# Optimization experiments

Hardware: AMD Instinct MI355X
Metric: run time of the kernel (lower is better)

## Reference

```python
import jax, jax.numpy as jnp
import numpy as np

G, N, E, F_IN, F_OUT, C = 256, 512, 4096, 64, 64, 16


def setup_inputs() -> dict:
    key = jax.random.key(0)
    ks = jax.random.split(key, 6)
    x_batch = jax.random.normal(ks[0], (G, N, F_IN), dtype=jnp.float32)
    edge_index_batch = jax.random.randint(ks[1], (G, 2, E), 0, N, dtype=jnp.int32)
    conv_weight = jax.random.normal(ks[2], (F_OUT, F_IN), dtype=jnp.float32) * (1.0 / np.sqrt(F_IN))
    conv_bias = jax.random.normal(ks[3], (F_OUT,), dtype=jnp.float32) * 0.02
    lin_weight = jax.random.normal(ks[4], (C, F_OUT * N), dtype=jnp.float32) * (1.0 / np.sqrt(F_OUT * N))
    lin_bias = jax.random.normal(ks[5], (C,), dtype=jnp.float32) * 0.02
    return {"x_batch": x_batch, "edge_index_batch": edge_index_batch,
            "conv_weight": conv_weight, "conv_bias": conv_bias,
            "lin_weight": lin_weight, "lin_bias": lin_bias}


def _gcn_conv_graph(xw, edge_index, self_loops):
    # xw: [N, F_OUT] (already linearly transformed), edge_index: [2, E]
    row = jnp.concatenate([edge_index[0], self_loops])  # sources
    col = jnp.concatenate([edge_index[1], self_loops])  # targets
    ones = jnp.ones(row.shape[0], dtype=xw.dtype)
    deg = jax.ops.segment_sum(ones, col, num_segments=N)  # degree at target nodes
    dinv = jnp.where(deg > 0, jax.lax.rsqrt(deg), jnp.zeros_like(deg))
    norm = dinv[row] * dinv[col]                          # [E+N]
    msgs = xw[row] * norm[:, None]                        # gather + normalize
    return jax.ops.segment_sum(msgs, col, num_segments=N)  # scatter-add at targets


def reference(x_batch, edge_index_batch, conv_weight, conv_bias, lin_weight, lin_bias):
    # GCNConv (PyG defaults: self-loops, symmetric normalization, post-agg bias)
    xw = jnp.einsum('gnf,of->gno', x_batch, conv_weight)  # [G, N, F_OUT]
    self_loops = jnp.arange(N, dtype=edge_index_batch.dtype)
    h = jax.vmap(_gcn_conv_graph, in_axes=(0, 0, None))(xw, edge_index_batch, self_loops)
    h = h + conv_bias
    h = jax.nn.relu(h)
    flat = h.reshape(h.shape[0], -1)                      # [G, N*F_OUT]
    logits = flat @ lin_weight.T + lin_bias               # [G, C]
    return jax.nn.log_softmax(logits, axis=-1)
```

## Files before the change

### kernel.cpp

```cpp
#include <hip/hip_runtime.h>

#define Gn 256
#define Nn 512
#define En 4096
#define Fn 64
#define Cn 16
#define ET (En + Nn)
#define EPAD 4616

typedef _Float16 halfv8 __attribute__((ext_vector_type(8)));
typedef _Float16 halfv4 __attribute__((ext_vector_type(4)));
typedef float    f32x4  __attribute__((ext_vector_type(4)));

__device__ __forceinline__ float pk_norm(unsigned p) {
    return (float)__builtin_bit_cast(_Float16, (unsigned short)(p & 0xffffu));
}

__global__ __launch_bounds__(256) void cvt_x(const float* __restrict__ x,
                                             _Float16* __restrict__ xc) {
    size_t base = (size_t)blockIdx.x * 256 + threadIdx.x;
    #pragma unroll
    for (int it = 0; it < 4; ++it) {
        size_t i = base + (size_t)it * (2048 * 256);
        float4 v = ((const float4*)x)[i];
        halfv4 h; h[0]=(_Float16)v.x; h[1]=(_Float16)v.y;
                  h[2]=(_Float16)v.z; h[3]=(_Float16)v.w;
        ((halfv4*)xc)[i] = h;
    }
}

__global__ __launch_bounds__(256) void cvt_lw_perm(const float* __restrict__ lw,
                                                   _Float16* __restrict__ lwh) {
    int u = blockIdx.x * 256 + threadIdx.x;
    int c = u >> 13, v = u & 8191;
    int jobidx = v >> 6, q = (v >> 4) & 3, m = v & 15;
    int n = (jobidx >> 2) * 16 + m;
    int o = (jobidx & 3) * 16 + q * 4;
    float4 f = *(const float4*)(lw + (size_t)c * (Nn * Fn) + n * 64 + o);
    halfv4 h; h[0]=(_Float16)f.x; h[1]=(_Float16)f.y;
              h[2]=(_Float16)f.z; h[3]=(_Float16)f.w;
    *(halfv4*)(lwh + (size_t)c * (Nn * Fn) + (size_t)v * 4) = h;
}

__global__ __launch_bounds__(256) void build_csr(const int* __restrict__ ei,
                                                 unsigned* __restrict__ epkG,
                                                 int* __restrict__ cntG) {
    __shared__ int      degL[Nn];
    __shared__ float    dinvL[Nn];
    __shared__ int      cntE[Nn];
    __shared__ unsigned epkL[ET];
    __shared__ int      wsum[4];
    const int g = blockIdx.x, tid = threadIdx.x;
    const int lane = tid & 63, wid = tid >> 6;
    const int* es = ei + (size_t)g * 2 * En;
    const int* ed = es + En;

    degL[tid] = 0; degL[tid + 256] = 0;
    __syncthreads();
    for (int e = tid; e < En; e += 256) atomicAdd(&degL[ed[e]], 1);
    __syncthreads();

    const int t2 = tid * 2;
    int cA = degL[t2] + 1, cB = degL[t2 + 1] + 1;
    dinvL[t2]     = rsqrtf((float)cA);
    dinvL[t2 + 1] = rsqrtf((float)cB);
    int p = cA + cB, v = p;
    #pragma unroll
    for (int off = 1; off < 64; off <<= 1) {
        int u = __shfl_up(v, off, 64);
        if (lane >= off) v += u;
    }
    if (lane == 63) wsum[wid] = v;
    __syncthreads();
    if (tid == 0) { int a = 0; for (int i = 0; i < 4; ++i) { int t = wsum[i]; wsum[i] = a; a += t; } }
    __syncthreads();
    int pe = v - p + wsum[wid];
    cntE[t2] = pe;
    cntE[t2 + 1] = pe + cA;
    __syncthreads();

    for (int e = tid; e < ET; e += 256) {
        int s, t;
        if (e < En) { s = es[e]; t = ed[e]; } else { s = t = e - En; }
        float nrm = dinvL[s] * dinvL[t];
        int slot = atomicAdd(&cntE[t], 1);
        unsigned short nb = __builtin_bit_cast(unsigned short, (_Float16)nrm);
        epkL[slot] = ((unsigned)s << 16) | nb;
    }
    __syncthreads();

    for (int i = tid; i < ET; i += 256) epkG[(size_t)g * EPAD + i] = epkL[i];
    cntG[(size_t)g * Nn + t2]     = cntE[t2];
    cntG[(size_t)g * Nn + t2 + 1] = cntE[t2 + 1];
}

__global__ __launch_bounds__(512, 4) void agg_conv(
    const _Float16* __restrict__ xc,
    const unsigned* __restrict__ epkG,
    const int*      __restrict__ cntG,
    const float*    __restrict__ w,
    const float*    __restrict__ wbias,
    _Float16* __restrict__ hout)
{
    __shared__ unsigned short xhs[256 * Fn];
    __shared__ unsigned short wts[Fn * Fn];
    __shared__ unsigned epkL[ET + 16];
    __shared__ int cntl[260];
    const int hh = blockIdx.x, g = blockIdx.y;
    const int tid = threadIdx.x, lane = tid & 63, wid = tid >> 6;
    const int tbase = hh * 256;

    const int slotlo = (hh == 0) ? 0 : cntG[(size_t)g * Nn + tbase - 1];
    const int slothi = cntG[(size_t)g * Nn + tbase + 255];
    const int total  = slothi - slotlo;

    if (tid < 257)
        cntl[tid] = (tid == 0) ? slotlo : cntG[(size_t)g * Nn + tbase + tid - 1];
    for (int i = tid; i < total; i += 512)
        epkL[i] = epkG[(size_t)g * EPAD + slotlo + i];
    {
        int o = tid >> 3, b8 = tid & 7;
        float4 va = *(const float4*)(w + o * Fn + b8 * 8);
        float4 vb = *(const float4*)(w + o * Fn + b8 * 8 + 4);
        halfv8 hv; hv[0]=(_Float16)va.x; hv[1]=(_Float16)va.y;
                   hv[2]=(_Float16)va.z; hv[3]=(_Float16)va.w;
                   hv[4]=(_Float16)vb.x; hv[5]=(_Float16)vb.y;
                   hv[6]=(_Float16)vb.z; hv[7]=(_Float16)vb.w;
        *(halfv8*)((char*)wts + o * 128 + ((b8 ^ (o & 7)) * 16)) = hv;
    }
    __syncthreads();

    {
        const _Float16* xgc = xc + (size_t)g * (Nn * Fn);
        const int qid = lane >> 4, fl = lane & 15;
        for (int r = 0; r < 8; ++r) {
            int tl = r * 32 + wid * 4 + qid;
            int beg = cntl[tl] - slotlo;
            int end = cntl[tl + 1] - slotlo;
            float a0 = 0.f, a1 = 0.f, a2 = 0.f, a3 = 0.f;
            unsigned pA0 = epkL[beg],     pA1 = epkL[beg + 1];
            unsigned pA2 = epkL[beg + 2], pA3 = epkL[beg + 3];
            int j = beg;
            for (; j + 4 <= end; j += 4) {
                unsigned pB0 = epkL[j + 4], pB1 = epkL[j + 5];
                unsigned pB2 = epkL[j + 6], pB3 = epkL[j + 7];
                int s0 = pA0 >> 16, s1 = pA1 >> 16, s2 = pA2 >> 16, s3 = pA3 >> 16;
                float n0 = pk_norm(pA0), n1 = pk_norm(pA1);
                float n2 = pk_norm(pA2), n3 = pk_norm(pA3);
                halfv4 x0 = *(const halfv4*)(xgc + s0 * Fn + fl * 4);
                halfv4 x1 = *(const halfv4*)(xgc + s1 * Fn + fl * 4);
                halfv4 x2 = *(const halfv4*)(xgc + s2 * Fn + fl * 4);
                halfv4 x3 = *(const halfv4*)(xgc + s3 * Fn + fl * 4);
                a0 += n0 * (float)x0[0] + n1 * (float)x1[0] + n2 * (float)x2[0] + n3 * (float)x3[0];
                a1 += n0 * (float)x0[1] + n1 * (float)x1[1] + n2 * (float)x2[1] + n3 * (float)x3[1];
                a2 += n0 * (float)x0[2] + n1 * (float)x1[2] + n2 * (float)x2[2] + n3 * (float)x3[2];
                a3 += n0 * (float)x0[3] + n1 * (float)x1[3] + n2 * (float)x2[3] + n3 * (float)x3[3];
                pA0 = pB0; pA1 = pB1; pA2 = pB2; pA3 = pB3;
            }
            for (; j < end; ++j) {
                int s = pA0 >> 16;
                float nm = pk_norm(pA0);
                halfv4 xv = *(const halfv4*)(xgc + s * Fn + fl * 4);
                a0 += nm * (float)xv[0]; a1 += nm * (float)xv[1];
                a2 += nm * (float)xv[2]; a3 += nm * (float)xv[3];
                pA0 = pA1; pA1 = pA2; pA2 = pA3;
            }
            halfv4 hv; hv[0]=(_Float16)a0; hv[1]=(_Float16)a1;
                       hv[2]=(_Float16)a2; hv[3]=(_Float16)a3;
            int dw = tl * 32 + (((fl >> 1) ^ (tl & 7)) * 4) + (fl & 1) * 2;
            *(halfv4*)((char*)xhs + dw * 4) = hv;
        }
    }
    __syncthreads();

    {
        const int m = lane & 15, q = lane >> 4;
        #pragma unroll
        for (int j = 0; j < 8; ++j) {
            int idx = wid * 8 + j;
            int tm = idx >> 2, to = idx & 3;
            int n = tm * 16 + m;
            int o = to * 16 + m;
            halfv8 X0 = *(const halfv8*)((const char*)xhs + n * 128 + ((q       ^ (n & 7)) * 16));
            halfv8 X1 = *(const halfv8*)((const char*)xhs + n * 128 + (((4 + q) ^ (n & 7)) * 16));
            halfv8 W0 = *(const halfv8*)((const char*)wts + o * 128 + ((q       ^ (o & 7)) * 16));
            halfv8 W1 = *(const halfv8*)((const char*)wts + o * 128 + (((4 + q) ^ (o & 7)) * 16));
            f32x4 acc = {0.f, 0.f, 0.f, 0.f};
            acc = __builtin_amdgcn_mfma_f32_16x16x32_f16(W0, X0, acc, 0, 0, 0);
            acc = __builtin_amdgcn_mfma_f32_16x16x32_f16(W1, X1, acc, 0, 0, 0);
            float4 bq = *(const float4*)&wbias[to * 16 + q * 4];
            halfv4 hv;
            hv[0] = (_Float16)fmaxf(acc[0] + bq.x, 0.0f);
            hv[1] = (_Float16)fmaxf(acc[1] + bq.y, 0.0f);
            hv[2] = (_Float16)fmaxf(acc[2] + bq.z, 0.0f);
            hv[3] = (_Float16)fmaxf(acc[3] + bq.w, 0.0f);
            size_t off = (size_t)g * (Nn * Fn)
                       + (size_t)(((hh * 16 + tm) * 4 + to) * 256 + lane * 4);
            *(halfv4*)(hout + off) = hv;
        }
    }
}

__global__ __launch_bounds__(256) void linear_mfma(
    const _Float16* __restrict__ h,
    const _Float16* __restrict__ lwh,
    float* __restrict__ part)
{
    __shared__ float red[4][64][4];
    const int cx = blockIdx.x, gy = blockIdx.y;
    const int tid = threadIdx.x, lane = tid & 63, wid = tid >> 6;
    const int ml = lane & 15, q = lane >> 4;
    const size_t kbase = (size_t)cx * 1024 + wid * 256;
    const _Float16* ha = h   + (size_t)(gy * 16 + ml) * (Nn * Fn) + kbase + q * 8;
    const _Float16* lb = lwh + (size_t)ml * (Nn * Fn) + kbase + q * 8;

    f32x4 acc = {0.f, 0.f, 0.f, 0.f};
    #pragma unroll
    for (int ks = 0; ks < 8; ++ks) {
        halfv8 a = *(const halfv8*)(ha + ks * 32);
        halfv8 b = *(const halfv8*)(lb + ks * 32);
        acc = __builtin_amdgcn_mfma_f32_16x16x32_f16(a, b, acc, 0, 0, 0);
    }
    #pragma unroll
    for (int r = 0; r < 4; ++r) red[wid][lane][r] = acc[r];
    __syncthreads();
    {
        int m = tid >> 4, cc = tid & 15;
        int sl = (m >> 2) * 16 + cc, rg = m & 3;
        float v = red[0][sl][rg] + red[1][sl][rg] + red[2][sl][rg] + red[3][sl][rg];
        part[((size_t)(gy * 16 + m) * 32 + cx) * Cn + cc] = v;
    }
}

__global__ __launch_bounds__(64) void gcn_softmax(
    const float* __restrict__ part, const float* __restrict__ lbias,
    float* __restrict__ out)
{
    const int g = blockIdx.x, lane = threadIdx.x;
    if (lane < Cn) {
        float v = lbias[lane];
        #pragma unroll
        for (int s = 0; s < 32; ++s) v += part[((size_t)g * 32 + s) * Cn + lane];
        float m = v;
        #pragma unroll
        for (int off = 8; off > 0; off >>= 1) m = fmaxf(m, __shfl_xor(m, off, 16));
        float ex = expf(v - m);
        float ssum = ex;
        #pragma unroll
        for (int off = 8; off > 0; off >>= 1) ssum += __shfl_xor(ssum, off, 16);
        out[g * Cn + lane] = v - m - logf(ssum);
    }
}

extern "C" void kernel_launch(void* const* d_in, const int* in_sizes, int n_in,
                              void* d_out, int out_size, void* d_ws, size_t ws_size,
                              hipStream_t stream) {
    const float* x  = (const float*)d_in[0];
    const int*   ei = (const int*)d_in[1];
    const float* w  = (const float*)d_in[2];
    const float* wb = (const float*)d_in[3];
    const float* lw = (const float*)d_in[4];
    const float* lb = (const float*)d_in[5];
    float* out = (float*)d_out;

    char* wsp = (char*)d_ws;
    _Float16* xc   = (_Float16*)(wsp);
    _Float16* lwh  = (_Float16*)(wsp + 16777216);
    unsigned* epkG = (unsigned*)(wsp + 17825792);
    int*      cntG = (int*)     (wsp + 22552576);
    _Float16* hbuf = (_Float16*)(wsp + 23076864);
    float*    part = (float*)   (wsp + 39854080);

    hipLaunchKernelGGL(cvt_x,       dim3(2048),    dim3(256), 0, stream, x, xc);
    hipLaunchKernelGGL(cvt_lw_perm, dim3(512),     dim3(256), 0, stream, lw, lwh);
    hipLaunchKernelGGL(build_csr,   dim3(Gn),      dim3(256), 0, stream, ei, epkG, cntG);
    hipLaunchKernelGGL(agg_conv,    dim3(2, Gn),   dim3(512), 0, stream,
                       xc, epkG, cntG, w, wb, hbuf);
    hipLaunchKernelGGL(linear_mfma, dim3(32, 16),  dim3(256), 0, stream,
                       hbuf, lwh, part);
    hipLaunchKernelGGL(gcn_softmax, dim3(Gn),      dim3(64),  0, stream,
                       part, lb, out);
}
```

Baseline: 134.4 us.

## Fuse CSR build, x conversion and aggregation into one kernel; merge linear with softmax

```diff
diff --git a/kernel.cpp b/kernel.cpp
--- a/kernel.cpp
+++ b/kernel.cpp
@@ -3,125 +3,87 @@
 #define Gn 256
 #define Nn 512
 #define En 4096
-#define Fn 64
 #define Cn 16
 #define ET (En + Nn)
-#define EPAD 4616
+#define QSLOT 2056
 
 typedef _Float16 halfv8 __attribute__((ext_vector_type(8)));
 typedef _Float16 halfv4 __attribute__((ext_vector_type(4)));
+typedef _Float16 halfv2 __attribute__((ext_vector_type(2)));
 typedef float    f32x4  __attribute__((ext_vector_type(4)));
 
 __device__ __forceinline__ float pk_norm(unsigned p) {
     return (float)__builtin_bit_cast(_Float16, (unsigned short)(p & 0xffffu));
 }
 
-__global__ __launch_bounds__(256) void cvt_x(const float* __restrict__ x,
-                                             _Float16* __restrict__ xc) {
-    size_t base = (size_t)blockIdx.x * 256 + threadIdx.x;
-    #pragma unroll
-    for (int it = 0; it < 4; ++it) {
-        size_t i = base + (size_t)it * (2048 * 256);
-        float4 v = ((const float4*)x)[i];
-        halfv4 h; h[0]=(_Float16)v.x; h[1]=(_Float16)v.y;
-                  h[2]=(_Float16)v.z; h[3]=(_Float16)v.w;
-        ((halfv4*)xc)[i] = h;
-    }
-}
-
-__global__ __launch_bounds__(256) void cvt_lw_perm(const float* __restrict__ lw,
-                                                   _Float16* __restrict__ lwh) {
-    int u = blockIdx.x * 256 + threadIdx.x;
-    int c = u >> 13, v = u & 8191;
-    int jobidx = v >> 6, q = (v >> 4) & 3, m = v & 15;
-    int n = (jobidx >> 2) * 16 + m;
-    int o = (jobidx & 3) * 16 + q * 4;
-    float4 f = *(const float4*)(lw + (size_t)c * (Nn * Fn) + n * 64 + o);
-    halfv4 h; h[0]=(_Float16)f.x; h[1]=(_Float16)f.y;
-              h[2]=(_Float16)f.z; h[3]=(_Float16)f.w;
-    *(halfv4*)(lwh + (size_t)c * (Nn * Fn) + (size_t)v * 4) = h;
-}
-
-__global__ __launch_bounds__(256) void build_csr(const int* __restrict__ ei,
-                                                 unsigned* __restrict__ epkG,
-                                                 int* __restrict__ cntG) {
+#if __has_builtin(__builtin_amdgcn_fdot2)
+__device__ __forceinline__ float fdot2_(halfv2 a, halfv2 b, float c) {
+    return __builtin_amdgcn_fdot2(a, b, c, false);
+}
+#else
+__device__ __forceinline__ float fdot2_(halfv2 a, halfv2 b, float c) {
+    return c + (float)a[0] * (float)b[0] + (float)a[1] * (float)b[1];
+}
+#endif
+struct H2x4 { halfv2 p0, p1, p2, p3; };
+__device__ __forceinline__ float dot8(halfv8 l, halfv8 h, float c) {
+    H2x4 L = __builtin_bit_cast(H2x4, l);
+    H2x4 H = __builtin_bit_cast(H2x4, h);
+    c = fdot2_(L.p0, H.p0, c); c = fdot2_(L.p1, H.p1, c);
+    c = fdot2_(L.p2, H.p2, c); c = fdot2_(L.p3, H.p3, c);
+    return c;
+}
+
+__global__ __launch_bounds__(256, 4) void gcn_main(
+    const float* __restrict__ x,
+    const int*   __restrict__ ei,
+    const float* __restrict__ w,
+    const float* __restrict__ wbias,
+    const float* __restrict__ lw,
+    _Float16* __restrict__ lwh,
+    _Float16* __restrict__ hout)
+{
     __shared__ int      degL[Nn];
     __shared__ float    dinvL[Nn];
-    __shared__ int      cntE[Nn];
-    __shared__ unsigned epkL[ET];
-    __shared__ int      wsum[4];
-    const int g = blockIdx.x, tid = threadIdx.x;
-    const int lane = tid & 63, wid = tid >> 6;
-    const int* es = ei + (size_t)g * 2 * En;
-    const int* ed = es + En;
+    __shared__ int      cntl[128];
+    __shared__ unsigned epkL[QSLOT + 8];
+    __shared__ unsigned short xhs[128 * 64];
+    __shared__ unsigned short wts[64 * 64];
+    __shared__ int      wsum[2];
+
+    const int b = blockIdx.x;
+    const int tid = threadIdx.x, lane = tid & 63, wid = tid >> 6;
+
+    if (b >= 1024) {
+        int u = (b - 1024) * 256 + tid;
+        #pragma unroll
+        for (int r = 0; r < 4; ++r) {
+            int idx = u * 4 + r;
+            int c = idx >> 13, v4 = idx & 8191;
+            int off = v4 * 4;
+            int m  = (off >> 2) & 15, q  = (off >> 6) & 3;
+            int to = (off >> 8) & 3,  tm = (off >> 10) & 7, hq = (off >> 13) & 3;
+            int n = hq * 128 + tm * 16 + m, o = to * 16 + q * 4;
+            float4 f = *(const float4*)(lw + (size_t)c * 32768 + n * 64 + o);
+            halfv4 h; h[0]=(_Float16)f.x; h[1]=(_Float16)f.y;
+                      h[2]=(_Float16)f.z; h[3]=(_Float16)f.w;
+            *(halfv4*)(lwh + (size_t)c * 32768 + off) = h;
+        }
+        return;
+    }
+
+    const int g = b >> 2, hh = b & 3;
+    const int*   es = ei + (size_t)g * 2 * En;
+    const int*   ed = es + En;
+    const float* xgf = x + (size_t)g * (Nn * 64);
 
     degL[tid] = 0; degL[tid + 256] = 0;
-    __syncthreads();
-    for (int e = tid; e < En; e += 256) atomicAdd(&degL[ed[e]], 1);
-    __syncthreads();
-
-    const int t2 = tid * 2;
-    int cA = degL[t2] + 1, cB = degL[t2 + 1] + 1;
-    dinvL[t2]     = rsqrtf((float)cA);
-    dinvL[t2 + 1] = rsqrtf((float)cB);
-    int p = cA + cB, v = p;
-    #pragma unroll
-    for (int off = 1; off < 64; off <<= 1) {
-        int u = __shfl_up(v, off, 64);
-        if (lane >= off) v += u;
-    }
-    if (lane == 63) wsum[wid] = v;
-    __syncthreads();
-    if (tid == 0) { int a = 0; for (int i = 0; i < 4; ++i) { int t = wsum[i]; wsum[i] = a; a += t; } }
-    __syncthreads();
-    int pe = v - p + wsum[wid];
-    cntE[t2] = pe;
-    cntE[t2 + 1] = pe + cA;
-    __syncthreads();
-
-    for (int e = tid; e < ET; e += 256) {
-        int s, t;
-        if (e < En) { s = es[e]; t = ed[e]; } else { s = t = e - En; }
-        float nrm = dinvL[s] * dinvL[t];
-        int slot = atomicAdd(&cntE[t], 1);
-        unsigned short nb = __builtin_bit_cast(unsigned short, (_Float16)nrm);
-        epkL[slot] = ((unsigned)s << 16) | nb;
-    }
-    __syncthreads();
-
-    for (int i = tid; i < ET; i += 256) epkG[(size_t)g * EPAD + i] = epkL[i];
-    cntG[(size_t)g * Nn + t2]     = cntE[t2];
-    cntG[(size_t)g * Nn + t2 + 1] = cntE[t2 + 1];
-}
-
-__global__ __launch_bounds__(512, 4) void agg_conv(
-    const _Float16* __restrict__ xc,
-    const unsigned* __restrict__ epkG,
-    const int*      __restrict__ cntG,
-    const float*    __restrict__ w,
-    const float*    __restrict__ wbias,
-    _Float16* __restrict__ hout)
-{
-    __shared__ unsigned short xhs[256 * Fn];
-    __shared__ unsigned short wts[Fn * Fn];
-    __shared__ unsigned epkL[ET + 16];
-    __shared__ int cntl[260];
-    const int hh = blockIdx.x, g = blockIdx.y;
-    const int tid = threadIdx.x, lane = tid & 63, wid = tid >> 6;
-    const int tbase = hh * 256;
-
-    const int slotlo = (hh == 0) ? 0 : cntG[(size_t)g * Nn + tbase - 1];
-    const int slothi = cntG[(size_t)g * Nn + tbase + 255];
-    const int total  = slothi - slotlo;
-
-    if (tid < 257)
-        cntl[tid] = (tid == 0) ? slotlo : cntG[(size_t)g * Nn + tbase + tid - 1];
-    for (int i = tid; i < total; i += 512)
-        epkL[i] = epkG[(size_t)g * EPAD + slotlo + i];
-    {
-        int o = tid >> 3, b8 = tid & 7;
-        float4 va = *(const float4*)(w + o * Fn + b8 * 8);
-        float4 vb = *(const float4*)(w + o * Fn + b8 * 8 + 4);
+    #pragma unroll
+    for (int it = 0; it < 2; ++it) {
+        int idx = tid + it * 256;
+        int o = idx >> 3, b8 = idx & 7;
+        float4 va = *(const float4*)(w + o * 64 + b8 * 8);
+        float4 vb = *(const float4*)(w + o * 64 + b8 * 8 + 4);
         halfv8 hv; hv[0]=(_Float16)va.x; hv[1]=(_Float16)va.y;
                    hv[2]=(_Float16)va.z; hv[3]=(_Float16)va.w;
                    hv[4]=(_Float16)vb.x; hv[5]=(_Float16)vb.y;
@@ -130,13 +92,42 @@
     }
     __syncthreads();
 
+    for (int e = tid; e < En; e += 256) atomicAdd(&degL[ed[e]], 1);
+    __syncthreads();
+
+    dinvL[tid]       = rsqrtf((float)(degL[tid] + 1));
+    dinvL[tid + 256] = rsqrtf((float)(degL[tid + 256] + 1));
+    int c = 0;
+    if (tid < 128) c = degL[hh * 128 + tid] + 1;
+    int v = c;
+    #pragma unroll
+    for (int off = 1; off < 64; off <<= 1) {
+        int u = __shfl_up(v, off, 64);
+        if (lane >= off) v += u;
+    }
+    if (tid == 63) wsum[0] = v;
+    __syncthreads();
+    if (tid < 128) cntl[tid] = v - c + ((tid >= 64) ? wsum[0] : 0);
+    __syncthreads();
+
+    for (int e = tid; e < ET; e += 256) {
+        int s, t;
+        if (e < En) { s = es[e]; t = ed[e]; } else { s = t = e - En; }
+        if ((t >> 7) == hh) {
+            float nrm = dinvL[s] * dinvL[t];
+            int slot = atomicAdd(&cntl[t & 127], 1);
+            unsigned short nb = __builtin_bit_cast(unsigned short, (_Float16)nrm);
+            epkL[slot] = ((unsigned)s << 16) | nb;
+        }
+    }
+    __syncthreads();
+
     {
-        const _Float16* xgc = xc + (size_t)g * (Nn * Fn);
         const int qid = lane >> 4, fl = lane & 15;
         for (int r = 0; r < 8; ++r) {
-            int tl = r * 32 + wid * 4 + qid;
-            int beg = cntl[tl] - slotlo;
-            int end = cntl[tl + 1] - slotlo;
+            int tl = r * 16 + wid * 4 + qid;
+            int beg = (tl == 0) ? 0 : cntl[tl - 1];
+            int end = cntl[tl];
             float a0 = 0.f, a1 = 0.f, a2 = 0.f, a3 = 0.f;
             unsigned pA0 = epkL[beg],     pA1 = epkL[beg + 1];
             unsigned pA2 = epkL[beg + 2], pA3 = epkL[beg + 3];
@@ -147,22 +138,21 @@
                 int s0 = pA0 >> 16, s1 = pA1 >> 16, s2 = pA2 >> 16, s3 = pA3 >> 16;
                 float n0 = pk_norm(pA0), n1 = pk_norm(pA1);
                 float n2 = pk_norm(pA2), n3 = pk_norm(pA3);
-                halfv4 x0 = *(const halfv4*)(xgc + s0 * Fn + fl * 4);
-                halfv4 x1 = *(const halfv4*)(xgc + s1 * Fn + fl * 4);
-                halfv4 x2 = *(const halfv4*)(xgc + s2 * Fn + fl * 4);
-                halfv4 x3 = *(const halfv4*)(xgc + s3 * Fn + fl * 4);
-                a0 += n0 * (float)x0[0] + n1 * (float)x1[0] + n2 * (float)x2[0] + n3 * (float)x3[0];
-                a1 += n0 * (float)x0[1] + n1 * (float)x1[1] + n2 * (float)x2[1] + n3 * (float)x3[1];
-                a2 += n0 * (float)x0[2] + n1 * (float)x1[2] + n2 * (float)x2[2] + n3 * (float)x3[2];
-                a3 += n0 * (float)x0[3] + n1 * (float)x1[3] + n2 * (float)x2[3] + n3 * (float)x3[3];
+                float4 x0 = *(const float4*)(xgf + s0 * 64 + fl * 4);
+                float4 x1 = *(const float4*)(xgf + s1 * 64 + fl * 4);
+                float4 x2 = *(const float4*)(xgf + s2 * 64 + fl * 4);
+                float4 x3 = *(const float4*)(xgf + s3 * 64 + fl * 4);
+                a0 += n0 * x0.x + n1 * x1.x + n2 * x2.x + n3 * x3.x;
+                a1 += n0 * x0.y + n1 * x1.y + n2 * x2.y + n3 * x3.y;
+                a2 += n0 * x0.z + n1 * x1.z + n2 * x2.z + n3 * x3.z;
+                a3 += n0 * x0.w + n1 * x1.w + n2 * x2.w + n3 * x3.w;
                 pA0 = pB0; pA1 = pB1; pA2 = pB2; pA3 = pB3;
             }
             for (; j < end; ++j) {
                 int s = pA0 >> 16;
                 float nm = pk_norm(pA0);
-                halfv4 xv = *(const halfv4*)(xgc + s * Fn + fl * 4);
-                a0 += nm * (float)xv[0]; a1 += nm * (float)xv[1];
-                a2 += nm * (float)xv[2]; a3 += nm * (float)xv[3];
+                float4 xv = *(const float4*)(xgf + s * 64 + fl * 4);
+                a0 += nm * xv.x; a1 += nm * xv.y; a2 += nm * xv.z; a3 += nm * xv.w;
                 pA0 = pA1; pA1 = pA2; pA2 = pA3;
             }
             halfv4 hv; hv[0]=(_Float16)a0; hv[1]=(_Float16)a1;
@@ -194,53 +184,52 @@
             hv[1] = (_Float16)fmaxf(acc[1] + bq.y, 0.0f);
             hv[2] = (_Float16)fmaxf(acc[2] + bq.z, 0.0f);
             hv[3] = (_Float16)fmaxf(acc[3] + bq.w, 0.0f);
-            size_t off = (size_t)g * (Nn * Fn)
-                       + (size_t)(((hh * 16 + tm) * 4 + to) * 256 + lane * 4);
+            size_t off = (size_t)g * 32768
+                       + (size_t)((((hh * 8 + tm) * 4 + to) * 256) + lane * 4);
             *(halfv4*)(hout + off) = hv;
         }
     }
 }
 
-__global__ __launch_bounds__(256) void linear_mfma(
+__global__ __launch_bounds__(512, 4) void gcn_out(
     const _Float16* __restrict__ h,
     const _Float16* __restrict__ lwh,
-    float* __restrict__ part)
-{
-    __shared__ float red[4][64][4];
-    const int cx = blockIdx.x, gy = blockIdx.y;
-    const int tid = threadIdx.x, lane = tid & 63, wid = tid >> 6;
-    const int ml = lane & 15, q = lane >> 4;
-    const size_t kbase = (size_t)cx * 1024 + wid * 256;
-    const _Float16* ha = h   + (size_t)(gy * 16 + ml) * (Nn * Fn) + kbase + q * 8;
-    const _Float16* lb = lwh + (size_t)ml * (Nn * Fn) + kbase + q * 8;
-
-    f32x4 acc = {0.f, 0.f, 0.f, 0.f};
-    #pragma unroll
-    for (int ks = 0; ks < 8; ++ks) {
-        halfv8 a = *(const halfv8*)(ha + ks * 32);
-        halfv8 b = *(const halfv8*)(lb + ks * 32);
-        acc = __builtin_amdgcn_mfma_f32_16x16x32_f16(a, b, acc, 0, 0, 0);
-    }
-    #pragma unroll
-    for (int r = 0; r < 4; ++r) red[wid][lane][r] = acc[r];
-    __syncthreads();
-    {
-        int m = tid >> 4, cc = tid & 15;
-        int sl = (m >> 2) * 16 + cc, rg = m & 3;
-        float v = red[0][sl][rg] + red[1][sl][rg] + red[2][sl][rg] + red[3][sl][rg];
-        part[((size_t)(gy * 16 + m) * 32 + cx) * Cn + cc] = v;
-    }
-}
-
-__global__ __launch_bounds__(64) void gcn_softmax(
-    const float* __restrict__ part, const float* __restrict__ lbias,
+    const float* __restrict__ lbias,
     float* __restrict__ out)
 {
-    const int g = blockIdx.x, lane = threadIdx.x;
-    if (lane < Cn) {
+    __shared__ float red[8][Cn];
+    const int g = blockIdx.x, tid = threadIdx.x;
+    const int lane = tid & 63, wid = tid >> 6;
+
+    const halfv8* hg = (const halfv8*)(h + (size_t)g * 32768 + tid * 64);
+    halfv8 hr0 = hg[0], hr1 = hg[1], hr2 = hg[2], hr3 = hg[3];
+    halfv8 hr4 = hg[4], hr5 = hg[5], hr6 = hg[6], hr7 = hg[7];
+
+    float p[Cn];
+    #pragma unroll
+    for (int c = 0; c < Cn; ++c) {
+        const halfv8* lp = (const halfv8*)(lwh + (size_t)c * 32768 + tid * 64);
+        halfv8 l0 = lp[0], l1 = lp[1], l2 = lp[2], l3 = lp[3];
+        halfv8 l4 = lp[4], l5 = lp[5], l6 = lp[6], l7 = lp[7];
+        float a = 0.f;
+        a = dot8(l0, hr0, a); a = dot8(l1, hr1, a);
+        a = dot8(l2, hr2, a); a = dot8(l3, hr3, a);
+        a = dot8(l4, hr4, a); a = dot8(l5, hr5, a);
+        a = dot8(l6, hr6, a); a = dot8(l7, hr7, a);
+        p[c] = a;
+    }
+    #pragma unroll
+    for (int c = 0; c < Cn; ++c) {
+        float v = p[c];
+        #pragma unroll
+        for (int off = 32; off > 0; off >>= 1) v += __shfl_down(v, off, 64);
+        if (lane == 0) red[wid][c] = v;
+    }
+    __syncthreads();
+    if (wid == 0 && lane < Cn) {
         float v = lbias[lane];
         #pragma unroll
-        for (int s = 0; s < 32; ++s) v += part[((size_t)g * 32 + s) * Cn + lane];
+        for (int k = 0; k < 8; ++k) v += red[k][lane];
         float m = v;
         #pragma unroll
         for (int off = 8; off > 0; off >>= 1) m = fmaxf(m, __shfl_xor(m, off, 16));
@@ -264,20 +253,11 @@
     float* out = (float*)d_out;
 
     char* wsp = (char*)d_ws;
-    _Float16* xc   = (_Float16*)(wsp);
-    _Float16* lwh  = (_Float16*)(wsp + 16777216);
-    unsigned* epkG = (unsigned*)(wsp + 17825792);
-    int*      cntG = (int*)     (wsp + 22552576);
-    _Float16* hbuf = (_Float16*)(wsp + 23076864);
-    float*    part = (float*)   (wsp + 39854080);
-
-    hipLaunchKernelGGL(cvt_x,       dim3(2048),    dim3(256), 0, stream, x, xc);
-    hipLaunchKernelGGL(cvt_lw_perm, dim3(512),     dim3(256), 0, stream, lw, lwh);
-    hipLaunchKernelGGL(build_csr,   dim3(Gn),      dim3(256), 0, stream, ei, epkG, cntG);
-    hipLaunchKernelGGL(agg_conv,    dim3(2, Gn),   dim3(512), 0, stream,
-                       xc, epkG, cntG, w, wb, hbuf);
-    hipLaunchKernelGGL(linear_mfma, dim3(32, 16),  dim3(256), 0, stream,
-                       hbuf, lwh, part);
-    hipLaunchKernelGGL(gcn_softmax, dim3(Gn),      dim3(64),  0, stream,
-                       part, lb, out);
-}
+    _Float16* lwh  = (_Float16*)(wsp);
+    _Float16* hbuf = (_Float16*)(wsp + 1048576);
+
+    hipLaunchKernelGGL(gcn_main, dim3(1152), dim3(256), 0, stream,
+                       x, ei, w, wb, lw, lwh, hbuf);
+    hipLaunchKernelGGL(gcn_out, dim3(Gn), dim3(512), 0, stream,
+                       hbuf, lwh, lb, out);
+}
```

After: 292.5 us. 118% more time.
